# Kernel optimization log

Measured on AMD Instinct MI355X. Metric: run time of the kernel, lower is better.

Reference implementation:

```python
import jax, jax.numpy as jnp
import numpy as np

B, T, E = 4, 2048, 2048
G, QG, D = 4, 4, 128  # kv groups, queries per group, head dim; H = G*QG = 16


def rope(x):
    # x: (..., T, D); rotate-half rotary positional embedding over the T axis
    t, d = x.shape[-2], x.shape[-1]
    half = d // 2
    inv_freq = 1.0 / (10000.0 ** (jnp.arange(half, dtype=jnp.float32) / half))
    ang = jnp.arange(t, dtype=jnp.float32)[:, None] * inv_freq[None, :]  # (T, half)
    cos, sin = jnp.cos(ang), jnp.sin(ang)
    x1, x2 = x[..., :half], x[..., half:]
    return jnp.concatenate([x1 * cos - x2 * sin, x1 * sin + x2 * cos], axis=-1)


def setup_inputs() -> dict:
    key = jax.random.key(0)
    ks = jax.random.split(key, 5)
    s = 0.02
    return {
        "x": jax.random.normal(ks[0], (B, T, E), dtype=jnp.float32),
        "Wq": jax.random.normal(ks[1], (E, G * QG * D), dtype=jnp.float32) * s,
        "Wk": jax.random.normal(ks[2], (E, G * D), dtype=jnp.float32) * s,
        "Wv": jax.random.normal(ks[3], (E, G * D), dtype=jnp.float32) * s,
        "Wo": jax.random.normal(ks[4], (G * QG * D, E), dtype=jnp.float32) * s,
    }


def reference(x, Wq, Wk, Wv, Wo):
    b, t, e = x.shape
    q = (x @ Wq).reshape(b, t, G, QG, D).transpose(0, 2, 3, 1, 4)  # (B,G,QG,T,D)
    k = (x @ Wk).reshape(b, t, G, D).transpose(0, 2, 1, 3)          # (B,G,T,D)
    v = (x @ Wv).reshape(b, t, G, D).transpose(0, 2, 1, 3)          # (B,G,T,D)
    q = rope(q)
    k = rope(k)
    scores = jnp.einsum("bgqtd,bgsd->bgqts", q, k) / jnp.sqrt(jnp.float32(D))
    causal = jnp.tril(jnp.ones((t, t), dtype=bool))                 # query t attends to s<=t
    scores = jnp.where(causal, scores, jnp.float32(-1e9))
    probs = jax.nn.softmax(scores, axis=-1)                         # (B,G,QG,T,T) explicit probs
    attn = jnp.einsum("bgqts,bgsd->bgqtd", probs, v)
    out = attn.transpose(0, 3, 1, 2, 4).reshape(b, t, G * QG * D)
    return out @ Wo
```

## Files before the change

### kernel.cpp

```cpp
#include <hip/hip_runtime.h>
#include <hip/hip_bf16.h>

typedef unsigned short u16;
typedef unsigned u32;
typedef float f32x4 __attribute__((ext_vector_type(4)));
typedef float f32x16 __attribute__((ext_vector_type(16)));
typedef short bf16x8 __attribute__((ext_vector_type(8)));

#define B_ 4
#define T_ 2048
#define E_ 2048
#define G_ 4
#define QG_ 4
#define D_ 128
#define H_ 16
#define BT_ 8192
#define SCALE2 0.12752745907f

__device__ __forceinline__ u16 f2bf(float f) {
  union { float f; unsigned u; } v; v.f = f;
  unsigned r = v.u + 0x7fffu + ((v.u >> 16) & 1u);
  return (u16)(r >> 16);
}
__device__ __forceinline__ float bf2f(u16 b) {
  union { unsigned u; float f; } v; v.u = ((unsigned)b) << 16;
  return v.f;
}
__device__ __forceinline__ unsigned packbf2(float lo, float hi) {
  __hip_bfloat162 h2 = __float22bfloat162_rn(make_float2(lo, hi));
  union { __hip_bfloat162 h; unsigned u; } cv; cv.h = h2; return cv.u;
}
#define EXP2F(x) __builtin_amdgcn_exp2f(x)

#define GL2LDS(g, l) __builtin_amdgcn_global_load_lds( \
    (const __attribute__((address_space(1))) void*)(g), \
    (__attribute__((address_space(3))) void*)(l), 16, 0, 0)

#define MFMA(a, b, c) __builtin_amdgcn_mfma_f32_16x16x32_bf16((a), (b), (c), 0, 0, 0)
#define MFMA32(a, b, c) __builtin_amdgcn_mfma_f32_32x32x16_bf16((a), (b), (c), 0, 0, 0)


__global__ void k_cvt_x(const float4* __restrict__ x, uint2* __restrict__ xb) {
  int i = blockIdx.x * 256 + threadIdx.x;
  float4 v = x[i];
  uint2 o;
  o.x = (unsigned)f2bf(v.x) | ((unsigned)f2bf(v.y) << 16);
  o.y = (unsigned)f2bf(v.z) | ((unsigned)f2bf(v.w) << 16);
  xb[i] = o;
}

__global__ void k_cvt_wT(const float* __restrict__ W, u16* __restrict__ WT,
                         int R, int C) {
  __shared__ float tile[64][65];
  int c0 = blockIdx.x * 64, r0 = blockIdx.y * 64;
  int tid = threadIdx.x;
#pragma unroll
  for (int p = 0; p < 16; ++p) {
    int idx = p * 256 + tid;
    int i = idx >> 6, j = idx & 63;
    tile[i][j] = W[(size_t)(r0 + i) * C + c0 + j];
  }
  __syncthreads();
#pragma unroll
  for (int p = 0; p < 16; ++p) {
    int idx = p * 256 + tid;
    int i = idx >> 6, j = idx & 63;
    WT[(size_t)(c0 + i) * R + r0 + j] = f2bf(tile[j][i]);
  }
}

__global__ void k_tables(float* __restrict__ ct, float* __restrict__ st) {
  int i = blockIdx.x * 256 + threadIdx.x;
  int t = i >> 6, j = i & 63;
  float freq = powf(10000.f, -(float)j / 64.f);
  float ang = (float)t * freq;
  ct[i] = cosf(ang);
  st[i] = sinf(ang);
}


__device__ __forceinline__ void rd_frag(bf16x8* dst, const u16* Xs,
                                        int r0, int r1, int r2, int r3,
                                        int lo, int hi) {
  int rows[4] = {r0, r1, r2, r3};
#pragma unroll
  for (int i = 0; i < 4; ++i) {
    int rw = rows[i] + lo;
    dst[i] = *(const bf16x8*)&Xs[(rw >> 1) * 64 +
        (((((rw & 1) << 2) | hi)) ^ ((rw >> 1) & 7)) * 8];
  }
}
__device__ __forceinline__ void mm16(f32x4 (*acc)[4], const bf16x8* a,
                                     const bf16x8* b) {
#pragma unroll
  for (int i = 0; i < 4; ++i)
#pragma unroll
    for (int j = 0; j < 4; ++j)
      acc[i][j] = MFMA(a[i], b[j], acc[i][j]);
}

template <int MODE>
__global__ __launch_bounds__(512, 2) void k_gemm256(
    const u16* __restrict__ A, const u16* __restrict__ Bt,
    void* __restrict__ C, const float* __restrict__ ct,
    const float* __restrict__ st, u16* __restrict__ kout,
    u16* __restrict__ vout, int M, int N, int K) {
  __shared__ u16 As[4][8192];
  __shared__ u16 Bs[4][8192];
  const int tid = threadIdx.x;
  const int wave = tid >> 6, lane = tid & 63;
  const int lo = lane & 15, hi = lane >> 4;
  const int nbn = N >> 8;
  const int bn = blockIdx.x % nbn;
  const int bm = blockIdx.x / nbn;
  const int m0 = bm * 256, n0 = bn * 256;
  const int wm = wave >> 2, wn = wave & 3;
  const int bbase = (MODE == 3) ? ((wn & 1) * 32 + (wn >> 1) * 128) : wn * 64;
  const int BO2 = (MODE == 3) ? 64 : 32;
  const int BO3 = (MODE == 3) ? 80 : 48;

  f32x4 acc[8][4] = {};

  auto stage = [&](const u16* __restrict__ X, int x0, u16* dstBase, int kcol) {
#pragma unroll
    for (int r = 0; r < 2; ++r) {
      int idx = r * 512 + tid;
      int pair = idx >> 3;
      int u = (idx & 7) ^ (pair & 7);
      GL2LDS(X + (size_t)(x0 + pair * 2 + (u >> 2)) * K + kcol + (u & 3) * 8,
             dstBase + (r * 512 + wave * 64) * 8);
    }
  };

  const int NT = K >> 6;
  stage(A, m0, &As[0][0], 0);
  stage(Bt, n0, &Bs[0][0], 0);
  stage(A, m0, &As[1][0], 32);
  stage(Bt, n0, &Bs[1][0], 32);
  asm volatile("s_waitcnt vmcnt(4)" ::: "memory");
  __builtin_amdgcn_s_barrier();

  for (int t = 0; t < NT; ++t) {
    const int s0 = (t & 1) << 1;
    const int sn = s0 ^ 2;
    const bool pf = (t + 1 < NT);
    const int kc = (t + 1) << 6;

    bf16x8 b0[4], b1[4], a[4];
    rd_frag(b0, &Bs[s0][0], bbase, bbase + 16, bbase + BO2, bbase + BO3, lo, hi);
    rd_frag(a, &As[s0][0], wm * 128, wm * 128 + 16, wm * 128 + 32, wm * 128 + 48, lo, hi);
    if (pf) stage(A, m0, &As[sn][0], kc);
    __builtin_amdgcn_s_barrier();
    __builtin_amdgcn_s_setprio(1);
    mm16(&acc[0], a, b0);
    __builtin_amdgcn_s_setprio(0);
    __builtin_amdgcn_s_barrier();
    rd_frag(a, &As[s0][0], wm * 128 + 64, wm * 128 + 80, wm * 128 + 96, wm * 128 + 112, lo, hi);
    if (pf) {
      stage(Bt, n0, &Bs[sn][0], kc);
      asm volatile("s_waitcnt vmcnt(4)" ::: "memory");
    } else {
      asm volatile("s_waitcnt vmcnt(0)" ::: "memory");
    }
    __builtin_amdgcn_s_barrier();
    __builtin_amdgcn_s_setprio(1);
    mm16(&acc[4], a, b0);
    __builtin_amdgcn_s_setprio(0);
    __builtin_amdgcn_s_barrier();
    rd_frag(b1, &Bs[s0 + 1][0], bbase, bbase + 16, bbase + BO2, bbase + BO3, lo, hi);
    rd_frag(a, &As[s0 + 1][0], wm * 128, wm * 128 + 16, wm * 128 + 32, wm * 128 + 48, lo, hi);
    if (pf) stage(A, m0, &As[sn + 1][0], kc + 32);
    __builtin_amdgcn_s_barrier();
    __builtin_amdgcn_s_setprio(1);
    mm16(&acc[0], a, b1);
    __builtin_amdgcn_s_setprio(0);
    __builtin_amdgcn_s_barrier();
    rd_frag(a, &As[s0 + 1][0], wm * 128 + 64, wm * 128 + 80, wm * 128 + 96, wm * 128 + 112, lo, hi);
    if (pf) {
      stage(Bt, n0, &Bs[sn + 1][0], kc + 32);
      asm volatile("s_waitcnt vmcnt(4)" ::: "memory");
    }
    __builtin_amdgcn_s_barrier();
    __builtin_amdgcn_s_setprio(1);
    mm16(&acc[4], a, b1);
    __builtin_amdgcn_s_setprio(0);
    __builtin_amdgcn_s_barrier();
  }

  if (MODE == 3) {
    if (bn >= 10) {
      const int n0v = n0 - 2560;
#pragma unroll
      for (int i = 0; i < 8; ++i)
#pragma unroll
        for (int j = 0; j < 4; ++j)
#pragma unroll
          for (int r = 0; r < 4; ++r) {
            int row = m0 + wm * 128 + i * 16 + hi * 4 + r;
            int col = n0v + bbase + (j & 1) * 16 + (j >> 1) * 64 + lo;
            vout[(size_t)row * 512 + col] = f2bf(acc[i][j][r]);
          }
    } else {
      const bool isq = (bn < 8);
      u16* out = isq ? (u16*)C : kout;
      const int hh = (isq ? (n0 >> 7) : ((n0 - 2048) >> 7)) + (wn >> 1);
      const int hbits = isq ? 4 : 2;
      const float sc = isq ? SCALE2 : 1.0f;
#pragma unroll
      for (int i = 0; i < 8; ++i)
#pragma unroll
        for (int r = 0; r < 4; ++r) {
          int rr = m0 + wm * 128 + i * 16 + hi * 4 + r;
          int bb = rr >> 11, tt = rr & (T_ - 1);
          size_t ro = ((size_t)((bb << hbits) + hh) * T_ + tt) << 7;
#pragma unroll
          for (int j = 0; j < 2; ++j) {
            int d1 = (wn & 1) * 32 + j * 16 + lo;
            float c = ct[tt * 64 + d1], s = st[tt * 64 + d1];
            float x1 = acc[i][j][r], x2 = acc[i][j + 2][r];
            out[ro + d1]      = f2bf((x1 * c - x2 * s) * sc);
            out[ro + d1 + 64] = f2bf((x1 * s + x2 * c) * sc);
          }
        }
    }
  } else {
#pragma unroll
    for (int i = 0; i < 8; ++i)
#pragma unroll
      for (int j = 0; j < 4; ++j)
#pragma unroll
        for (int r = 0; r < 4; ++r) {
          int row = m0 + wm * 128 + i * 16 + hi * 4 + r;
          int col = n0 + wn * 64 + j * 16 + lo;
          ((float*)C)[(size_t)row * N + col] = acc[i][j][r];
        }
  }
}

__global__ void k_vtrans(const u16* __restrict__ vg, u16* __restrict__ vT,
                         int sstr) {
  __shared__ u16 tile[64][65];
  int t0 = blockIdx.x * 64;
  int d0 = blockIdx.y * 64;
  int bg = blockIdx.z;
  int g = bg & (G_ - 1), b = bg >> 2;
  int tid = threadIdx.x;
#pragma unroll
  for (int p = 0; p < 16; ++p) {
    int idx = p * 256 + tid;
    int i = idx >> 6, j = idx & 63;
    tile[i][j] = vg[(size_t)(b * T_ + t0 + i) * sstr + g * D_ + d0 + j];
  }
  __syncthreads();
#pragma unroll
  for (int p = 0; p < 16; ++p) {
    int idx = p * 256 + tid;
    int i = idx >> 6, j = idx & 63;
    vT[((size_t)bg * D_ + d0 + i) * T_ + t0 + j] = tile[j][i];
  }
}


__device__ __forceinline__ void swap32(u32 a, u32 b, u32& x, u32& y) {
#if __has_builtin(__builtin_amdgcn_permlane32_swap)
  auto rr = __builtin_amdgcn_permlane32_swap(a, b, false, false);
  x = rr[0]; y = rr[1];
#else
  u32 as = __shfl_xor(a, 32), bs = __shfl_xor(b, 32);
  int hi = (threadIdx.x & 63) >> 5;
  x = hi ? bs : a;
  y = hi ? b : as;
#endif
}

__global__ __launch_bounds__(256, 2) void k_attn(
    const u16* __restrict__ qh, const u16* __restrict__ kh,
    const u16* __restrict__ vT, u16* __restrict__ ab) {
  __shared__ u16 Ks[2][64 * 128];
  __shared__ u16 Vs[2][128 * 64];
  const int tid = threadIdx.x;
  const int wave = tid >> 6;
  const int lane = tid & 63;
  const int l5 = lane & 31, h1 = lane >> 5;

  const int f = blockIdx.x;
  const int xcd = f & 7;
  const int slot = f >> 3;
  const int bg = xcd * 2 + (slot & 1);
  const int rest = slot >> 1;
  const int qg = rest & 3;
  const int i0 = (15 - (rest >> 2)) * 128;
  const int b = bg >> 2, g = bg & 3;
  const int h = g * 4 + qg;
  const int bh = b * 16 + h;

  const int qw0 = i0 + wave * 32;
  const int q = qw0 + l5;

  const u16* Qrow = qh + ((size_t)bh * T_ + q) * D_;
  bf16x8 qf[8];
#pragma unroll
  for (int kk = 0; kk < 8; ++kk)
    qf[kk] = *(const bf16x8*)(Qrow + kk * 16 + h1 * 8);

  const u16* Kbase = kh + (size_t)(b * G_ + g) * T_ * D_;
  const u16* Vbase = vT + (size_t)(b * G_ + g) * D_ * T_;

  auto stage = [&](int bi, int s0) {
#pragma unroll
    for (int r = 0; r < 4; ++r) {
      int p = r * 256 + tid;
      {
        int row = p >> 4, c = p & 15;
        GL2LDS(Kbase + (size_t)(s0 + row) * D_ + ((c ^ (row & 15)) * 8),
               &Ks[bi][(r * 256 + wave * 64) * 8]);
      }
      {
        int row = p >> 3, c = p & 7;
        GL2LDS(Vbase + (size_t)row * T_ + s0 + ((c ^ (row & 7)) * 8),
               &Vs[bi][(r * 256 + wave * 64) * 8]);
      }
    }
  };

  bf16x8 onesf;
#pragma unroll
  for (int i = 0; i < 8; ++i) onesf[i] = (short)0x3F80;

  f32x16 acc[4] = {};
  f32x16 accS = {};

  const int nt = ((i0 + 127) >> 6) + 1;
  stage(0, 0);
  int bufc = 0;
  for (int ti = 0; ti < nt; ++ti) {
    const int s0 = ti << 6;
    __syncthreads();
    if (ti + 1 < nt) stage(bufc ^ 1, (ti + 1) << 6);
    if (s0 <= qw0 + 31) {
      f32x16 sa[2] = {};
#pragma unroll
      for (int st = 0; st < 2; ++st) {
        if (s0 + st * 32 <= qw0 + 31) {
#pragma unroll
          for (int kk = 0; kk < 8; ++kk) {
            int row = st * 32 + l5;
            bf16x8 kf = *(const bf16x8*)
                &Ks[bufc][row * 128 + ((2 * kk + h1) ^ (row & 15)) * 8];
            sa[st] = MFMA32(kf, qf[kk], sa[st]);
          }
        }
      }
#pragma unroll
      for (int st = 0; st < 2; ++st) {
        const bool needm = (s0 + st * 32 + 31 > qw0);
        if (needm) {
#pragma unroll
          for (int r = 0; r < 16; ++r) {
            int s = s0 + st * 32 + (r & 3) + 8 * (r >> 2) + 4 * h1;
            if (s > q) sa[st][r] = -1e9f;
          }
        }
      }
      bf16x8 pf[4];
#pragma unroll
      for (int st = 0; st < 2; ++st) {
        float pe[16];
#pragma unroll
        for (int r = 0; r < 16; ++r) pe[r] = EXP2F(sa[st][r]);
#pragma unroll
        for (int kl = 0; kl < 2; ++kl) {
          u32 w0 = packbf2(pe[kl * 8 + 0], pe[kl * 8 + 1]);
          u32 w1 = packbf2(pe[kl * 8 + 2], pe[kl * 8 + 3]);
          u32 y0 = packbf2(pe[kl * 8 + 4], pe[kl * 8 + 5]);
          u32 y1 = packbf2(pe[kl * 8 + 6], pe[kl * 8 + 7]);
          union { u32 w[4]; bf16x8 v; } pw;
          swap32(w0, y0, pw.w[0], pw.w[2]);
          swap32(w1, y1, pw.w[1], pw.w[3]);
          pf[st * 2 + kl] = pw.v;
        }
      }
#pragma unroll
      for (int ks = 0; ks < 4; ++ks) {
#pragma unroll
        for (int dt = 0; dt < 4; ++dt) {
          int row = dt * 32 + l5;
          bf16x8 vf = *(const bf16x8*)
              &Vs[bufc][row * 64 + ((2 * ks + h1) ^ (row & 7)) * 8];
          acc[dt] = MFMA32(vf, pf[ks], acc[dt]);
        }
        accS = MFMA32(onesf, pf[ks], accS);
      }
    }
    bufc ^= 1;
  }
  const float iv = 1.f / accS[0];
  u16* outrow = ab + ((size_t)(b * T_ + q)) * (H_ * D_) + (size_t)h * D_;
#pragma unroll
  for (int dt = 0; dt < 4; ++dt)
#pragma unroll
    for (int g4 = 0; g4 < 4; ++g4) {
      uint2 o;
      o.x = (u32)f2bf(acc[dt][g4 * 4 + 0] * iv) |
            ((u32)f2bf(acc[dt][g4 * 4 + 1] * iv) << 16);
      o.y = (u32)f2bf(acc[dt][g4 * 4 + 2] * iv) |
            ((u32)f2bf(acc[dt][g4 * 4 + 3] * iv) << 16);
      *(uint2*)(outrow + dt * 32 + 8 * g4 + 4 * h1) = o;
    }
}


extern "C" void kernel_launch(void* const* d_in, const int* in_sizes, int n_in,
                              void* d_out, int out_size, void* d_ws, size_t ws_size,
                              hipStream_t stream) {
  const float* x  = (const float*)d_in[0];
  const float* Wq = (const float*)d_in[1];
  const float* Wk = (const float*)d_in[2];
  const float* Wv = (const float*)d_in[3];
  const float* Wo = (const float*)d_in[4];

  char* base = (char*)d_ws;
  size_t off = 0;
  auto nxt = [&](size_t bytes) {
    char* r = base + off;
    off += (bytes + 255) & ~(size_t)255;
    return r;
  };
  u16*   xb   = (u16*)nxt((size_t)BT_ * E_ * 2);
  u16*   wAll = (u16*)nxt((size_t)3072 * E_ * 2);
  u16*   woT  = (u16*)nxt((size_t)E_ * E_ * 2);
  float* ct   = (float*)nxt((size_t)T_ * 64 * 4);
  float* st   = (float*)nxt((size_t)T_ * 64 * 4);
  u16*   qhb  = (u16*)nxt((size_t)BT_ * E_ * 2);
  u16*   khb  = (u16*)nxt((size_t)BT_ * (G_ * D_) * 2);
  u16*   vg   = (u16*)nxt((size_t)BT_ * (G_ * D_) * 2);
  u16*   vTb  = (u16*)nxt((size_t)BT_ * (G_ * D_) * 2);
  u16* ab = xb;

  k_cvt_x<<<BT_ * E_ / 4 / 256, 256, 0, stream>>>((const float4*)x, (uint2*)xb);
  k_cvt_wT<<<dim3(E_ / 64, E_ / 64), 256, 0, stream>>>(Wq, wAll, E_, E_);
  k_cvt_wT<<<dim3((G_ * D_) / 64, E_ / 64), 256, 0, stream>>>(
      Wk, wAll + (size_t)2048 * E_, E_, G_ * D_);
  k_cvt_wT<<<dim3((G_ * D_) / 64, E_ / 64), 256, 0, stream>>>(
      Wv, wAll + (size_t)2560 * E_, E_, G_ * D_);
  k_cvt_wT<<<dim3(E_ / 64, E_ / 64), 256, 0, stream>>>(Wo, woT, E_, E_);
  k_tables<<<T_ * 64 / 256, 256, 0, stream>>>(ct, st);

  k_gemm256<3><<<dim3((3072 / 256) * (BT_ / 256)), 512, 0, stream>>>(
      xb, wAll, qhb, ct, st, khb, vg, BT_, 3072, E_);

  k_vtrans<<<dim3(T_ / 64, D_ / 64, B_ * G_), 256, 0, stream>>>(vg, vTb, 512);

  k_attn<<<dim3(1024), 256, 0, stream>>>(qhb, khb, vTb, ab);

  k_gemm256<0><<<dim3((E_ / 256) * (BT_ / 256)), 512, 0, stream>>>(
      ab, woT, d_out, nullptr, nullptr, nullptr, nullptr, BT_, E_, E_);
}
```

Baseline: 316.9 us.

## Process 256 query rows per attention block and sum probabilities with shuffles

Each attention block now covers 256 queries instead of 128, with every wave handling two 32-row query halves against the same staged K/V tile, so the grid shrinks to 512 blocks and each K/V tile load is reused twice as much. The row-sum MFMA against a ones vector is replaced by a register reduction plus a cross-half shuffle. Q fragments are reloaded from global memory every tile rather than kept in registers. This halves global K/V traffic but doubles accumulator registers, lowers block count for load balance across CUs, and adds repeated Q reads.

```diff
diff --git a/kernel.cpp b/kernel.cpp
--- a/kernel.cpp
+++ b/kernel.cpp
@@ -289,22 +289,16 @@
   const int bg = xcd * 2 + (slot & 1);
   const int rest = slot >> 1;
   const int qg = rest & 3;
-  const int i0 = (15 - (rest >> 2)) * 128;
+  const int i0 = (7 - (rest >> 2)) * 256;
   const int b = bg >> 2, g = bg & 3;
   const int h = g * 4 + qg;
   const int bh = b * 16 + h;
 
-  const int qw0 = i0 + wave * 32;
-  const int q = qw0 + l5;
-
-  const u16* Qrow = qh + ((size_t)bh * T_ + q) * D_;
-  bf16x8 qf[8];
-#pragma unroll
-  for (int kk = 0; kk < 8; ++kk)
-    qf[kk] = *(const bf16x8*)(Qrow + kk * 16 + h1 * 8);
+  const int qw0 = i0 + wave * 64;
 
   const u16* Kbase = kh + (size_t)(b * G_ + g) * T_ * D_;
   const u16* Vbase = vT + (size_t)(b * G_ + g) * D_ * T_;
+  const u16* Qbase = qh + (size_t)bh * T_ * D_;
 
   auto stage = [&](int bi, int s0) {
 #pragma unroll
@@ -323,90 +317,111 @@
     }
   };
 
-  bf16x8 onesf;
-#pragma unroll
-  for (int i = 0; i < 8; ++i) onesf[i] = (short)0x3F80;
-
-  f32x16 acc[4] = {};
-  f32x16 accS = {};
-
-  const int nt = ((i0 + 127) >> 6) + 1;
+  f32x16 acc2[2][4] = {};
+  float lrun[2] = {0.f, 0.f};
+
+  const int nt = (i0 >> 6) + 4;
   stage(0, 0);
   int bufc = 0;
   for (int ti = 0; ti < nt; ++ti) {
     const int s0 = ti << 6;
     __syncthreads();
     if (ti + 1 < nt) stage(bufc ^ 1, (ti + 1) << 6);
-    if (s0 <= qw0 + 31) {
-      f32x16 sa[2] = {};
-#pragma unroll
-      for (int st = 0; st < 2; ++st) {
-        if (s0 + st * 32 <= qw0 + 31) {
-#pragma unroll
-          for (int kk = 0; kk < 8; ++kk) {
-            int row = st * 32 + l5;
-            bf16x8 kf = *(const bf16x8*)
-                &Ks[bufc][row * 128 + ((2 * kk + h1) ^ (row & 15)) * 8];
-            sa[st] = MFMA32(kf, qf[kk], sa[st]);
+    if (s0 <= qw0 + 63) {
+#pragma unroll
+      for (int hq = 0; hq < 2; ++hq) {
+        const int qh0 = qw0 + hq * 32;
+        if (s0 <= qh0 + 31) {
+          const int q = qh0 + l5;
+          const u16* Qrow = Qbase + (size_t)q * D_;
+          bf16x8 qf[8];
+#pragma unroll
+          for (int kk = 0; kk < 8; ++kk)
+            qf[kk] = *(const bf16x8*)(Qrow + kk * 16 + h1 * 8);
+          f32x16 sa[2] = {};
+#pragma unroll
+          for (int st = 0; st < 2; ++st) {
+            if (s0 + st * 32 <= qh0 + 31) {
+#pragma unroll
+              for (int kk = 0; kk < 8; ++kk) {
+                int row = st * 32 + l5;
+                bf16x8 kf = *(const bf16x8*)
+                    &Ks[bufc][row * 128 + ((2 * kk + h1) ^ (row & 15)) * 8];
+                sa[st] = MFMA32(kf, qf[kk], sa[st]);
+              }
+            }
+          }
+#pragma unroll
+          for (int st = 0; st < 2; ++st) {
+            const bool needm = (s0 + st * 32 + 31 > qh0);
+            if (needm) {
+#pragma unroll
+              for (int r = 0; r < 16; ++r) {
+                int s = s0 + st * 32 + (r & 3) + 8 * (r >> 2) + 4 * h1;
+                if (s > q) sa[st][r] = -1e9f;
+              }
+            }
+          }
+          bf16x8 pf[4];
+          float se[16];
+#pragma unroll
+          for (int st = 0; st < 2; ++st) {
+            float pe[16];
+#pragma unroll
+            for (int r = 0; r < 16; ++r) {
+              pe[r] = EXP2F(sa[st][r]);
+              if (st == 0) se[r] = pe[r]; else se[r] += pe[r];
+            }
+#pragma unroll
+            for (int kl = 0; kl < 2; ++kl) {
+              u32 w0 = packbf2(pe[kl * 8 + 0], pe[kl * 8 + 1]);
+              u32 w1 = packbf2(pe[kl * 8 + 2], pe[kl * 8 + 3]);
+              u32 y0 = packbf2(pe[kl * 8 + 4], pe[kl * 8 + 5]);
+              u32 y1 = packbf2(pe[kl * 8 + 6], pe[kl * 8 + 7]);
+              union { u32 w[4]; bf16x8 v; } pw;
+              swap32(w0, y0, pw.w[0], pw.w[2]);
+              swap32(w1, y1, pw.w[1], pw.w[3]);
+              pf[st * 2 + kl] = pw.v;
+            }
+          }
+#pragma unroll
+          for (int off = 8; off >= 1; off >>= 1)
+#pragma unroll
+            for (int r = 0; r < 8; ++r)
+              if (r < off) se[r] += se[r + off];
+          lrun[hq] += se[0] + __shfl_xor(se[0], 32);
+#pragma unroll
+          for (int ks = 0; ks < 4; ++ks) {
+#pragma unroll
+            for (int dt = 0; dt < 4; ++dt) {
+              int row = dt * 32 + l5;
+              bf16x8 vf = *(const bf16x8*)
+                  &Vs[bufc][row * 64 + ((2 * ks + h1) ^ (row & 7)) * 8];
+              acc2[hq][dt] = MFMA32(vf, pf[ks], acc2[hq][dt]);
+            }
           }
         }
       }
-#pragma unroll
-      for (int st = 0; st < 2; ++st) {
-        const bool needm = (s0 + st * 32 + 31 > qw0);
-        if (needm) {
-#pragma unroll
-          for (int r = 0; r < 16; ++r) {
-            int s = s0 + st * 32 + (r & 3) + 8 * (r >> 2) + 4 * h1;
-            if (s > q) sa[st][r] = -1e9f;
-          }
-        }
+    }
+    bufc ^= 1;
+  }
+#pragma unroll
+  for (int hq = 0; hq < 2; ++hq) {
+    const float iv = 1.f / lrun[hq];
+    const int q = qw0 + hq * 32 + l5;
+    u16* outrow = ab + ((size_t)(b * T_ + q)) * (H_ * D_) + (size_t)h * D_;
+#pragma unroll
+    for (int dt = 0; dt < 4; ++dt)
+#pragma unroll
+      for (int g4 = 0; g4 < 4; ++g4) {
+        uint2 o;
+        o.x = (u32)f2bf(acc2[hq][dt][g4 * 4 + 0] * iv) |
+              ((u32)f2bf(acc2[hq][dt][g4 * 4 + 1] * iv) << 16);
+        o.y = (u32)f2bf(acc2[hq][dt][g4 * 4 + 2] * iv) |
+              ((u32)f2bf(acc2[hq][dt][g4 * 4 + 3] * iv) << 16);
+        *(uint2*)(outrow + dt * 32 + 8 * g4 + 4 * h1) = o;
       }
-      bf16x8 pf[4];
-#pragma unroll
-      for (int st = 0; st < 2; ++st) {
-        float pe[16];
-#pragma unroll
-        for (int r = 0; r < 16; ++r) pe[r] = EXP2F(sa[st][r]);
-#pragma unroll
-        for (int kl = 0; kl < 2; ++kl) {
-          u32 w0 = packbf2(pe[kl * 8 + 0], pe[kl * 8 + 1]);
-          u32 w1 = packbf2(pe[kl * 8 + 2], pe[kl * 8 + 3]);
-          u32 y0 = packbf2(pe[kl * 8 + 4], pe[kl * 8 + 5]);
-          u32 y1 = packbf2(pe[kl * 8 + 6], pe[kl * 8 + 7]);
-          union { u32 w[4]; bf16x8 v; } pw;
-          swap32(w0, y0, pw.w[0], pw.w[2]);
-          swap32(w1, y1, pw.w[1], pw.w[3]);
-          pf[st * 2 + kl] = pw.v;
-        }
-      }
-#pragma unroll
-      for (int ks = 0; ks < 4; ++ks) {
-#pragma unroll
-        for (int dt = 0; dt < 4; ++dt) {
-          int row = dt * 32 + l5;
-          bf16x8 vf = *(const bf16x8*)
-              &Vs[bufc][row * 64 + ((2 * ks + h1) ^ (row & 7)) * 8];
-          acc[dt] = MFMA32(vf, pf[ks], acc[dt]);
-        }
-        accS = MFMA32(onesf, pf[ks], accS);
-      }
-    }
-    bufc ^= 1;
-  }
-  const float iv = 1.f / accS[0];
-  u16* outrow = ab + ((size_t)(b * T_ + q)) * (H_ * D_) + (size_t)h * D_;
-#pragma unroll
-  for (int dt = 0; dt < 4; ++dt)
-#pragma unroll
-    for (int g4 = 0; g4 < 4; ++g4) {
-      uint2 o;
-      o.x = (u32)f2bf(acc[dt][g4 * 4 + 0] * iv) |
-            ((u32)f2bf(acc[dt][g4 * 4 + 1] * iv) << 16);
-      o.y = (u32)f2bf(acc[dt][g4 * 4 + 2] * iv) |
-            ((u32)f2bf(acc[dt][g4 * 4 + 3] * iv) << 16);
-      *(uint2*)(outrow + dt * 32 + 8 * g4 + 4 * h1) = o;
-    }
+  }
 }
 
 
@@ -451,7 +466,7 @@
 
   k_vtrans<<<dim3(T_ / 64, D_ / 64, B_ * G_), 256, 0, stream>>>(vg, vTb, 512);
 
-  k_attn<<<dim3(1024), 256, 0, stream>>>(qhb, khb, vTb, ab);
+  k_attn<<<dim3(512), 256, 0, stream>>>(qhb, khb, vTb, ab);
 
   k_gemm256<0><<<dim3((E_ / 256) * (BT_ / 256)), 512, 0, stream>>>(
       ab, woT, d_out, nullptr, nullptr, nullptr, nullptr, BT_, E_, E_);
```

After: 405.0 us. 1.28x slower.
